# Performance work log

Measured on AMD Instinct MI355X. Metric: run time of the kernel, lower is better.

## Reference

```python
import jax, jax.numpy as jnp
import numpy as np

LN_EPS = 1e-5

def _layernorm(x, g, b):
    mu = jnp.mean(x, axis=-1, keepdims=True)
    var = jnp.var(x, axis=-1, keepdims=True)
    return (x - mu) * jax.lax.rsqrt(var + LN_EPS) * g + b

def setup_inputs() -> dict:
    key = jax.random.key(0)
    ks = jax.random.split(key, 8)
    B, N, C, OUT, H = 2, 512, 256, 256, 4
    s_in = 1.0 / np.sqrt(C)
    s_2c = 1.0 / np.sqrt(2 * C)
    s_out = 1.0 / np.sqrt(OUT)
    return {
        "x": jax.random.normal(ks[0], (B, N, C), jnp.float32),
        "We": jax.random.uniform(ks[1], (2 * C, OUT), jnp.float32, -s_2c, s_2c),
        "be": jnp.zeros((OUT,), jnp.float32),
        "ln1_g": jnp.ones((OUT,), jnp.float32),
        "ln1_b": jnp.zeros((OUT,), jnp.float32),
        "W2": jax.random.uniform(ks[2], (OUT, H), jnp.float32, -s_out, s_out),
        "b2": jnp.zeros((H,), jnp.float32),
        "Wv": jax.random.uniform(ks[3], (C, OUT), jnp.float32, -s_in, s_in),
        "bv": jnp.zeros((OUT,), jnp.float32),
        "Wo": jax.random.uniform(ks[4], (OUT, OUT), jnp.float32, -s_out, s_out),
        "bo": jnp.zeros((OUT,), jnp.float32),
        "ln2_g": jnp.ones((OUT,), jnp.float32),
        "ln2_b": jnp.zeros((OUT,), jnp.float32),
    }

def reference(x, We, be, ln1_g, ln1_b, W2, b2, Wv, bv, Wo, bo, ln2_g, ln2_b):
    B, N, C = x.shape
    OUT = We.shape[1]
    H = W2.shape[1]
    hd = OUT // H
    # edge MLP first Linear on concat([x_i, x_j]) == x_i@We[:C] + x_j@We[C:] + be
    h_i = x @ We[:C] + be          # [B,N,OUT]
    h_j = x @ We[C:]               # [B,N,OUT]
    e = h_i[:, :, None, :] + h_j[:, None, :, :]   # [B,Ni,Nj,OUT]
    e = jax.nn.gelu(_layernorm(e, ln1_g, ln1_b), approximate=False)
    logits = e @ W2 + b2                           # [B,Ni,Nj,H]
    adj = jax.nn.softmax(logits, axis=2)           # softmax over Nj
    v = (x @ Wv + bv).reshape(B, N, H, hd)         # [B,N,H,hd]
    out = jnp.einsum('bijh,bjhd->bihd', adj, v).reshape(B, N, OUT)
    out = out @ Wo + bo
    return _layernorm(out + x, ln2_g, ln2_b)
```

## Files before the change

kernel.cpp:

```cpp
#include <hip/hip_runtime.h>
#include <math.h>

#define NB    2
#define NN    512
#define CC    256
#define OUTC  256
#define HH    4
#define LN_EPS 1e-5f

__device__ __forceinline__ float gelu_fast(float x) {
    float s   = x * x;
    float w   = fmaf(-0.1029432f, s, -2.3022077f);
    float e   = exp2f(x * w);
    return x * __builtin_amdgcn_rcpf(1.0f + e);
}

__global__ __launch_bounds__(256) void kA(
    const float* __restrict__ x,  const float* __restrict__ We,
    const float* __restrict__ be, const float* __restrict__ Wv,
    const float* __restrict__ bv,
    float* __restrict__ hi, float* __restrict__ hj, float* __restrict__ v)
{
    __shared__ __align__(16) float xs[4][CC];
    const int r0 = blockIdx.x * 4;
    const int t  = threadIdx.x;
    #pragma unroll
    for (int k = 0; k < 4; ++k)
        xs[k][t] = x[(size_t)(r0 + k) * CC + t];
    __syncthreads();

    float ai[4] = {0,0,0,0}, aj[4] = {0,0,0,0}, av[4] = {0,0,0,0};
    for (int c = 0; c < CC; ++c) {
        float we0 = We[(size_t)c * OUTC + t];
        float we1 = We[(size_t)(CC + c) * OUTC + t];
        float wv  = Wv[(size_t)c * OUTC + t];
        #pragma unroll
        for (int k = 0; k < 4; ++k) {
            float xv = xs[k][c];
            ai[k] = fmaf(xv, we0, ai[k]);
            aj[k] = fmaf(xv, we1, aj[k]);
            av[k] = fmaf(xv, wv , av[k]);
        }
    }
    float beT = be[t], bvT = bv[t];
    #pragma unroll
    for (int k = 0; k < 4; ++k) {
        hi[(size_t)(r0 + k) * OUTC + t] = ai[k] + beT;
        hj[(size_t)(r0 + k) * OUTC + t] = aj[k];
        v [(size_t)(r0 + k) * OUTC + t] = av[k] + bvT;
    }
}

#define LDP 260
__global__ __launch_bounds__(256) void kB(
    const float* __restrict__ hi,  const float* __restrict__ hj,
    const float* __restrict__ ln1g, const float* __restrict__ ln1b,
    const float* __restrict__ W2,  const float* __restrict__ b2,
    float* __restrict__ logits)
{
    __shared__ __align__(16) float hjs[32][LDP];
    __shared__ __align__(16) float his[8][LDP];
    __shared__ __align__(16) float g1s[CC];
    __shared__ __align__(16) float b1s[CC];
    __shared__ __align__(16) float w2s[CC][HH];

    const int bid = blockIdx.x;
    const int jt  = (bid & 15) * 32;
    const int it  = ((bid >> 4) & 63) * 8;
    const int b   = bid >> 10;
    const int t   = threadIdx.x;

    {
        const float4* src = (const float4*)(hj + (size_t)(b * NN + jt) * OUTC);
        #pragma unroll
        for (int k = 0; k < 8; ++k) {
            int s   = k * 256 + t;
            int row = s >> 6, c4 = s & 63;
            *(float4*)&hjs[row][c4 * 4] = src[s];
        }
    }
    {
        const float4* src = (const float4*)(hi + (size_t)(b * NN + it) * OUTC);
        #pragma unroll
        for (int k = 0; k < 2; ++k) {
            int s   = k * 256 + t;
            int row = s >> 6, c4 = s & 63;
            *(float4*)&his[row][c4 * 4] = src[s];
        }
    }
    g1s[t] = ln1g[t];
    b1s[t] = ln1b[t];
    #pragma unroll
    for (int k = 0; k < 4; ++k)
        ((float*)w2s)[t + 256 * k] = W2[t + 256 * k];
    __syncthreads();

    const int w = t >> 6, l = t & 63;
    const int i = it + 2 * w + (l >> 5);
    const int j = jt + (l & 31);
    const float* __restrict__ hirow = &his[2 * w + (l >> 5)][0];
    const float* __restrict__ hjrow = &hjs[l & 31][0];

    float s = 0.f, ss = 0.f;
    #pragma unroll 4
    for (int c4 = 0; c4 < 64; ++c4) {
        float4 a  = *(const float4*)&hirow[c4 * 4];
        float4 bb = *(const float4*)&hjrow[c4 * 4];
        float e0 = a.x + bb.x, e1 = a.y + bb.y, e2 = a.z + bb.z, e3 = a.w + bb.w;
        s += (e0 + e1) + (e2 + e3);
        ss = fmaf(e0, e0, ss); ss = fmaf(e1, e1, ss);
        ss = fmaf(e2, e2, ss); ss = fmaf(e3, e3, ss);
    }
    const float mu  = s * (1.f / 256.f);
    const float var = fmaf(ss, 1.f / 256.f, -mu * mu);
    const float rs  = rsqrtf(var + LN_EPS);
    const float nmurs = -mu * rs;

    float p0 = 0.f, p1 = 0.f, p2 = 0.f, p3 = 0.f;
    #pragma unroll 4
    for (int c4 = 0; c4 < 64; ++c4) {
        float4 a  = *(const float4*)&hirow[c4 * 4];
        float4 bb = *(const float4*)&hjrow[c4 * 4];
        float4 g  = ((const float4*)g1s)[c4];
        float4 be_ = ((const float4*)b1s)[c4];
        const float4* w2r = (const float4*)&w2s[c4 * 4][0];
        {
            float n = fmaf(a.x + bb.x, rs, nmurs);
            n = fmaf(n, g.x, be_.x);
            float ge = gelu_fast(n);
            float4 wr = w2r[0];
            p0 = fmaf(ge, wr.x, p0); p1 = fmaf(ge, wr.y, p1);
            p2 = fmaf(ge, wr.z, p2); p3 = fmaf(ge, wr.w, p3);
        }
        {
            float n = fmaf(a.y + bb.y, rs, nmurs);
            n = fmaf(n, g.y, be_.y);
            float ge = gelu_fast(n);
            float4 wr = w2r[1];
            p0 = fmaf(ge, wr.x, p0); p1 = fmaf(ge, wr.y, p1);
            p2 = fmaf(ge, wr.z, p2); p3 = fmaf(ge, wr.w, p3);
        }
        {
            float n = fmaf(a.z + bb.z, rs, nmurs);
            n = fmaf(n, g.z, be_.z);
            float ge = gelu_fast(n);
            float4 wr = w2r[2];
            p0 = fmaf(ge, wr.x, p0); p1 = fmaf(ge, wr.y, p1);
            p2 = fmaf(ge, wr.z, p2); p3 = fmaf(ge, wr.w, p3);
        }
        {
            float n = fmaf(a.w + bb.w, rs, nmurs);
            n = fmaf(n, g.w, be_.w);
            float ge = gelu_fast(n);
            float4 wr = w2r[3];
            p0 = fmaf(ge, wr.x, p0); p1 = fmaf(ge, wr.y, p1);
            p2 = fmaf(ge, wr.z, p2); p3 = fmaf(ge, wr.w, p3);
        }
    }
    float4 b2v = *(const float4*)b2;
    float4 outv = make_float4(p0 + b2v.x, p1 + b2v.y, p2 + b2v.z, p3 + b2v.w);
    ((float4*)logits)[(size_t)(b * NN + i) * NN + j] = outv;
}

__global__ __launch_bounds__(256) void kC(
    const float* __restrict__ logits, const float* __restrict__ v,
    const float* __restrict__ Wo,     const float* __restrict__ bo,
    const float* __restrict__ x,      const float* __restrict__ g2,
    const float* __restrict__ b2ln,   float* __restrict__ out)
{
    __shared__ __align__(16) float wl[4 * NN * HH];
    __shared__ __align__(16) float sm[4][HH][2];
    __shared__ __align__(16) float out1[4][OUTC];
    __shared__ float redb[4][4][2];

    const int bid = blockIdx.x;
    const int b   = bid >> 7;
    const int it  = (bid & 127) * 4;
    const int t   = threadIdx.x;

    {
        const float4* src = (const float4*)logits + (size_t)(b * NN + it) * NN;
        float4* dst = (float4*)wl;
        #pragma unroll
        for (int k = 0; k < 8; ++k) dst[t + 256 * k] = src[t + 256 * k];
    }
    __syncthreads();

    {
        const int g = t >> 4, k = t & 15;
        const int i = g >> 2, h = g & 3;
        const float* base = wl + i * (NN * HH) + h;
        float m = -1e30f;
        for (int jj = 0; jj < 32; ++jj) m = fmaxf(m, base[(k * 32 + jj) * 4]);
        #pragma unroll
        for (int off = 1; off < 16; off <<= 1) m = fmaxf(m, __shfl_xor(m, off));
        float ssum = 0.f;
        for (int jj = 0; jj < 32; ++jj) ssum += __expf(base[(k * 32 + jj) * 4] - m);
        #pragma unroll
        for (int off = 1; off < 16; off <<= 1) ssum += __shfl_xor(ssum, off);
        if (k == 0) { sm[i][h][0] = m; sm[i][h][1] = 1.f / ssum; }
    }
    __syncthreads();

    {
        #pragma unroll 4
        for (int k = 0; k < 32; ++k) {
            int idx = t + 256 * k;
            int i = idx >> 11, h = idx & 3;
            wl[idx] = __expf(wl[idx] - sm[i][h][0]) * sm[i][h][1];
        }
    }
    __syncthreads();

    {
        const int h = t >> 6;
        float a0 = 0.f, a1 = 0.f, a2 = 0.f, a3 = 0.f;
        const float* vb = v + (size_t)b * NN * OUTC + t;
        for (int j = 0; j < NN; ++j) {
            float vv = vb[(size_t)j * OUTC];
            a0 = fmaf(wl[0 * 2048 + j * 4 + h], vv, a0);
            a1 = fmaf(wl[1 * 2048 + j * 4 + h], vv, a1);
            a2 = fmaf(wl[2 * 2048 + j * 4 + h], vv, a2);
            a3 = fmaf(wl[3 * 2048 + j * 4 + h], vv, a3);
        }
        out1[0][t] = a0; out1[1][t] = a1; out1[2][t] = a2; out1[3][t] = a3;
    }
    __syncthreads();

    {
        float a0 = bo[t], a1 = a0, a2 = a0, a3 = a0;
        for (int c = 0; c < OUTC; ++c) {
            float wv = Wo[(size_t)c * OUTC + t];
            a0 = fmaf(out1[0][c], wv, a0);
            a1 = fmaf(out1[1][c], wv, a1);
            a2 = fmaf(out1[2][c], wv, a2);
            a3 = fmaf(out1[3][c], wv, a3);
        }
        float r[4];
        r[0] = a0 + x[(size_t)(b * NN + it + 0) * OUTC + t];
        r[1] = a1 + x[(size_t)(b * NN + it + 1) * OUTC + t];
        r[2] = a2 + x[(size_t)(b * NN + it + 2) * OUTC + t];
        r[3] = a3 + x[(size_t)(b * NN + it + 3) * OUTC + t];

        const int w = t >> 6, l = t & 63;
        #pragma unroll
        for (int i = 0; i < 4; ++i) {
            float sv = r[i], sq = r[i] * r[i];
            #pragma unroll
            for (int off = 1; off < 64; off <<= 1) {
                sv += __shfl_xor(sv, off);
                sq += __shfl_xor(sq, off);
            }
            if (l == 0) { redb[w][i][0] = sv; redb[w][i][1] = sq; }
        }
        __syncthreads();
        float gg = g2[t], bb = b2ln[t];
        #pragma unroll
        for (int i = 0; i < 4; ++i) {
            float sv = redb[0][i][0] + redb[1][i][0] + redb[2][i][0] + redb[3][i][0];
            float sq = redb[0][i][1] + redb[1][i][1] + redb[2][i][1] + redb[3][i][1];
            float mu  = sv * (1.f / 256.f);
            float var = sq * (1.f / 256.f) - mu * mu;
            float rsi = rsqrtf(var + LN_EPS);
            out[(size_t)(b * NN + it + i) * OUTC + t] = (r[i] - mu) * rsi * gg + bb;
        }
    }
}

extern "C" void kernel_launch(void* const* d_in, const int* in_sizes, int n_in,
                              void* d_out, int out_size, void* d_ws, size_t ws_size,
                              hipStream_t stream) {
    (void)in_sizes; (void)n_in; (void)out_size; (void)ws_size;
    const float* x    = (const float*)d_in[0];
    const float* We   = (const float*)d_in[1];
    const float* be   = (const float*)d_in[2];
    const float* ln1g = (const float*)d_in[3];
    const float* ln1b = (const float*)d_in[4];
    const float* W2   = (const float*)d_in[5];
    const float* b2   = (const float*)d_in[6];
    const float* Wv   = (const float*)d_in[7];
    const float* bv   = (const float*)d_in[8];
    const float* Wo   = (const float*)d_in[9];
    const float* bo   = (const float*)d_in[10];
    const float* ln2g = (const float*)d_in[11];
    const float* ln2b = (const float*)d_in[12];
    float* out = (float*)d_out;

    float* ws = (float*)d_ws;
    float* hi     = ws;
    float* hj     = ws + 262144;
    float* v      = ws + 524288;
    float* logits = ws + 786432;

    kA<<<256,  256, 0, stream>>>(x, We, be, Wv, bv, hi, hj, v);
    kB<<<2048, 256, 0, stream>>>(hi, hj, ln1g, ln1b, W2, b2, logits);
    kC<<<256,  256, 0, stream>>>(logits, v, Wo, bo, x, ln2g, ln2b, out);
}
```

Measured before the change: 224.5 us.

## Decompose edge LayerNorm statistics into per-node sums plus cross dot-product kernel

The first-pass LayerNorm statistics in the edge kernel are no longer computed over all 256 channels per (i,j) pair. They are rebuilt algebraically from per-node sums and squared sums, emitted by kA, plus an hi·hj cross term produced by a new tiled dot-product kernel kX. This removes one full 256-wide pass per edge, at the cost of an extra launch, an extra workspace round trip, and possible cancellation in E[x^2]-mu^2. kA is also rewritten to give each wave one row with float4 weight loads, and kC now handles 2 rows per block so it launches twice as many blocks.

```diff
diff --git a/kernel.cpp b/kernel.cpp
--- a/kernel.cpp
+++ b/kernel.cpp
@@ -8,10 +8,20 @@
 #define HH    4
 #define LN_EPS 1e-5f
 
+#define WS_HI     0
+#define WS_HJ     262144
+#define WS_V      524288
+#define WS_LOGITS 786432
+#define WS_CROSS  2883584
+#define WS_SI     3407872
+#define WS_SSI    3408896
+#define WS_SJ     3409920
+#define WS_SSJ    3410944
+
 __device__ __forceinline__ float gelu_fast(float x) {
-    float s   = x * x;
-    float w   = fmaf(-0.1029432f, s, -2.3022077f);
-    float e   = exp2f(x * w);
+    float s = x * x;
+    float w = fmaf(-0.1029432f, s, -2.3022077f);
+    float e = exp2f(x * w);
     return x * __builtin_amdgcn_rcpf(1.0f + e);
 }
 
@@ -19,7 +29,9 @@
     const float* __restrict__ x,  const float* __restrict__ We,
     const float* __restrict__ be, const float* __restrict__ Wv,
     const float* __restrict__ bv,
-    float* __restrict__ hi, float* __restrict__ hj, float* __restrict__ v)
+    float* __restrict__ hi, float* __restrict__ hj, float* __restrict__ v,
+    float* __restrict__ Si, float* __restrict__ SSi,
+    float* __restrict__ Sj, float* __restrict__ SSj)
 {
     __shared__ __align__(16) float xs[4][CC];
     const int r0 = blockIdx.x * 4;
@@ -29,26 +41,97 @@
         xs[k][t] = x[(size_t)(r0 + k) * CC + t];
     __syncthreads();
 
-    float ai[4] = {0,0,0,0}, aj[4] = {0,0,0,0}, av[4] = {0,0,0,0};
+    const int w = t >> 6, l = t & 63;
+    const int r = r0 + w;
+    const float* __restrict__ xrow = xs[w];
+    const float4* __restrict__ We0 = (const float4*)We + l;
+    const float4* __restrict__ We1 = (const float4*)(We + (size_t)CC * OUTC) + l;
+    const float4* __restrict__ Wv4 = (const float4*)Wv + l;
+
+    float4 ai = {0,0,0,0}, aj = {0,0,0,0}, av = {0,0,0,0};
+    #pragma unroll 4
     for (int c = 0; c < CC; ++c) {
-        float we0 = We[(size_t)c * OUTC + t];
-        float we1 = We[(size_t)(CC + c) * OUTC + t];
-        float wv  = Wv[(size_t)c * OUTC + t];
-        #pragma unroll
-        for (int k = 0; k < 4; ++k) {
-            float xv = xs[k][c];
-            ai[k] = fmaf(xv, we0, ai[k]);
-            aj[k] = fmaf(xv, we1, aj[k]);
-            av[k] = fmaf(xv, wv , av[k]);
-        }
-    }
-    float beT = be[t], bvT = bv[t];
+        float xv = xrow[c];
+        float4 a = We0[(size_t)c * 64];
+        float4 bq = We1[(size_t)c * 64];
+        float4 cq = Wv4[(size_t)c * 64];
+        ai.x = fmaf(xv, a.x, ai.x); ai.y = fmaf(xv, a.y, ai.y);
+        ai.z = fmaf(xv, a.z, ai.z); ai.w = fmaf(xv, a.w, ai.w);
+        aj.x = fmaf(xv, bq.x, aj.x); aj.y = fmaf(xv, bq.y, aj.y);
+        aj.z = fmaf(xv, bq.z, aj.z); aj.w = fmaf(xv, bq.w, aj.w);
+        av.x = fmaf(xv, cq.x, av.x); av.y = fmaf(xv, cq.y, av.y);
+        av.z = fmaf(xv, cq.z, av.z); av.w = fmaf(xv, cq.w, av.w);
+    }
+    float4 be4 = ((const float4*)be)[l];
+    float4 bv4 = ((const float4*)bv)[l];
+    float4 hiv = make_float4(ai.x + be4.x, ai.y + be4.y, ai.z + be4.z, ai.w + be4.w);
+    float4 vv  = make_float4(av.x + bv4.x, av.y + bv4.y, av.z + bv4.z, av.w + bv4.w);
+
+    ((float4*)hi)[(size_t)r * 64 + l] = hiv;
+    ((float4*)hj)[(size_t)r * 64 + l] = aj;
+    ((float4*)v )[(size_t)r * 64 + l] = vv;
+
+    float si = (hiv.x + hiv.y) + (hiv.z + hiv.w);
+    float ssi = hiv.x * hiv.x;
+    ssi = fmaf(hiv.y, hiv.y, ssi); ssi = fmaf(hiv.z, hiv.z, ssi); ssi = fmaf(hiv.w, hiv.w, ssi);
+    float sj = (aj.x + aj.y) + (aj.z + aj.w);
+    float ssj = aj.x * aj.x;
+    ssj = fmaf(aj.y, aj.y, ssj); ssj = fmaf(aj.z, aj.z, ssj); ssj = fmaf(aj.w, aj.w, ssj);
     #pragma unroll
-    for (int k = 0; k < 4; ++k) {
-        hi[(size_t)(r0 + k) * OUTC + t] = ai[k] + beT;
-        hj[(size_t)(r0 + k) * OUTC + t] = aj[k];
-        v [(size_t)(r0 + k) * OUTC + t] = av[k] + bvT;
-    }
+    for (int off = 1; off < 64; off <<= 1) {
+        si  += __shfl_xor(si,  off);
+        ssi += __shfl_xor(ssi, off);
+        sj  += __shfl_xor(sj,  off);
+        ssj += __shfl_xor(ssj, off);
+    }
+    if (l == 0) { Si[r] = si; SSi[r] = ssi; Sj[r] = sj; SSj[r] = ssj; }
+}
+
+#define LXP 260
+__global__ __launch_bounds__(256) void kX(
+    const float* __restrict__ hi, const float* __restrict__ hj,
+    float* __restrict__ cross)
+{
+    __shared__ __align__(16) float his[32][LXP];
+    __shared__ __align__(16) float hjs[32][LXP];
+    const int bid = blockIdx.x;
+    const int b  = bid >> 8;
+    const int i0 = ((bid >> 4) & 15) * 32;
+    const int j0 = (bid & 15) * 32;
+    const int t  = threadIdx.x;
+
+    const float4* srcA = (const float4*)(hi + ((size_t)b * NN + i0) * OUTC);
+    const float4* srcB = (const float4*)(hj + ((size_t)b * NN + j0) * OUTC);
+    #pragma unroll
+    for (int k = 0; k < 8; ++k) {
+        int s = k * 256 + t, row = s >> 6, c4 = s & 63;
+        *(float4*)&his[row][c4 * 4] = srcA[s];
+        *(float4*)&hjs[row][c4 * 4] = srcB[s];
+    }
+    __syncthreads();
+
+    const int oi = (t & 15) * 2, oj = (t >> 4) * 2;
+    float a00 = 0.f, a01 = 0.f, a10 = 0.f, a11 = 0.f;
+    #pragma unroll 2
+    for (int c4 = 0; c4 < 64; ++c4) {
+        float4 A0 = *(const float4*)&his[oi    ][c4 * 4];
+        float4 A1 = *(const float4*)&his[oi + 1][c4 * 4];
+        float4 B0 = *(const float4*)&hjs[oj    ][c4 * 4];
+        float4 B1 = *(const float4*)&hjs[oj + 1][c4 * 4];
+        a00 = fmaf(A0.x, B0.x, a00); a00 = fmaf(A0.y, B0.y, a00);
+        a00 = fmaf(A0.z, B0.z, a00); a00 = fmaf(A0.w, B0.w, a00);
+        a01 = fmaf(A0.x, B1.x, a01); a01 = fmaf(A0.y, B1.y, a01);
+        a01 = fmaf(A0.z, B1.z, a01); a01 = fmaf(A0.w, B1.w, a01);
+        a10 = fmaf(A1.x, B0.x, a10); a10 = fmaf(A1.y, B0.y, a10);
+        a10 = fmaf(A1.z, B0.z, a10); a10 = fmaf(A1.w, B0.w, a10);
+        a11 = fmaf(A1.x, B1.x, a11); a11 = fmaf(A1.y, B1.y, a11);
+        a11 = fmaf(A1.z, B1.z, a11); a11 = fmaf(A1.w, B1.w, a11);
+    }
+    size_t base = ((size_t)b * NN + i0 + oi) * NN + j0 + oj;
+    cross[base]          = a00;
+    cross[base + 1]      = a01;
+    cross[base + NN]     = a10;
+    cross[base + NN + 1] = a11;
 }
 
 #define LDP 260
@@ -56,6 +139,9 @@
     const float* __restrict__ hi,  const float* __restrict__ hj,
     const float* __restrict__ ln1g, const float* __restrict__ ln1b,
     const float* __restrict__ W2,  const float* __restrict__ b2,
+    const float* __restrict__ Si,  const float* __restrict__ SSi,
+    const float* __restrict__ Sj,  const float* __restrict__ SSj,
+    const float* __restrict__ cross,
     float* __restrict__ logits)
 {
     __shared__ __align__(16) float hjs[32][LDP];
@@ -63,6 +149,8 @@
     __shared__ __align__(16) float g1s[CC];
     __shared__ __align__(16) float b1s[CC];
     __shared__ __align__(16) float w2s[CC][HH];
+    __shared__ __align__(16) float crs[256];
+    __shared__ float sis[8], ssis[8], sjs[32], ssjs[32];
 
     const int bid = blockIdx.x;
     const int jt  = (bid & 15) * 32;
@@ -74,8 +162,7 @@
         const float4* src = (const float4*)(hj + (size_t)(b * NN + jt) * OUTC);
         #pragma unroll
         for (int k = 0; k < 8; ++k) {
-            int s   = k * 256 + t;
-            int row = s >> 6, c4 = s & 63;
+            int s = k * 256 + t, row = s >> 6, c4 = s & 63;
             *(float4*)&hjs[row][c4 * 4] = src[s];
         }
     }
@@ -83,8 +170,7 @@
         const float4* src = (const float4*)(hi + (size_t)(b * NN + it) * OUTC);
         #pragma unroll
         for (int k = 0; k < 2; ++k) {
-            int s   = k * 256 + t;
-            int row = s >> 6, c4 = s & 63;
+            int s = k * 256 + t, row = s >> 6, c4 = s & 63;
             *(float4*)&his[row][c4 * 4] = src[s];
         }
     }
@@ -93,26 +179,22 @@
     #pragma unroll
     for (int k = 0; k < 4; ++k)
         ((float*)w2s)[t + 256 * k] = W2[t + 256 * k];
+    crs[t] = cross[((size_t)(b * NN + it + (t >> 5))) * NN + jt + (t & 31)];
+    if (t < 8)               { sis[t] = Si[b * NN + it + t];  ssis[t] = SSi[b * NN + it + t]; }
+    if (t >= 64 && t < 96)   { int q = t - 64; sjs[q] = Sj[b * NN + jt + q]; ssjs[q] = SSj[b * NN + jt + q]; }
     __syncthreads();
 
     const int w = t >> 6, l = t & 63;
-    const int i = it + 2 * w + (l >> 5);
-    const int j = jt + (l & 31);
-    const float* __restrict__ hirow = &his[2 * w + (l >> 5)][0];
-    const float* __restrict__ hjrow = &hjs[l & 31][0];
-
-    float s = 0.f, ss = 0.f;
-    #pragma unroll 4
-    for (int c4 = 0; c4 < 64; ++c4) {
-        float4 a  = *(const float4*)&hirow[c4 * 4];
-        float4 bb = *(const float4*)&hjrow[c4 * 4];
-        float e0 = a.x + bb.x, e1 = a.y + bb.y, e2 = a.z + bb.z, e3 = a.w + bb.w;
-        s += (e0 + e1) + (e2 + e3);
-        ss = fmaf(e0, e0, ss); ss = fmaf(e1, e1, ss);
-        ss = fmaf(e2, e2, ss); ss = fmaf(e3, e3, ss);
-    }
-    const float mu  = s * (1.f / 256.f);
-    const float var = fmaf(ss, 1.f / 256.f, -mu * mu);
+    const int il = 2 * w + (l >> 5);
+    const int jl = l & 31;
+    const int i = it + il;
+    const int j = jt + jl;
+    const float* __restrict__ hirow = &his[il][0];
+    const float* __restrict__ hjrow = &hjs[jl][0];
+
+    const float mu  = (sis[il] + sjs[jl]) * (1.f / 256.f);
+    const float msq = fmaf(2.f, crs[(il << 5) + jl], ssis[il] + ssjs[jl]) * (1.f / 256.f);
+    const float var = fmaf(-mu, mu, msq);
     const float rs  = rsqrtf(var + LN_EPS);
     const float nmurs = -mu * rs;
 
@@ -168,101 +250,108 @@
     const float* __restrict__ x,      const float* __restrict__ g2,
     const float* __restrict__ b2ln,   float* __restrict__ out)
 {
-    __shared__ __align__(16) float wl[4 * NN * HH];
-    __shared__ __align__(16) float sm[4][HH][2];
-    __shared__ __align__(16) float out1[4][OUTC];
-    __shared__ float redb[4][4][2];
+    __shared__ __align__(16) float wl[2][NN * HH];
+    __shared__ __align__(16) float sm[2][HH][2];
+    __shared__ __align__(16) float out1[2][OUTC];
+    __shared__ float redb[4][2][2];
 
     const int bid = blockIdx.x;
-    const int b   = bid >> 7;
-    const int it  = (bid & 127) * 4;
+    const int b   = bid >> 8;
+    const int i0  = (bid & 255) * 2;
     const int t   = threadIdx.x;
 
     {
-        const float4* src = (const float4*)logits + (size_t)(b * NN + it) * NN;
+        const float4* src = (const float4*)(logits + ((size_t)b * NN + i0) * NN * HH);
         float4* dst = (float4*)wl;
         #pragma unroll
-        for (int k = 0; k < 8; ++k) dst[t + 256 * k] = src[t + 256 * k];
-    }
-    __syncthreads();
-
-    {
-        const int g = t >> 4, k = t & 15;
-        const int i = g >> 2, h = g & 3;
-        const float* base = wl + i * (NN * HH) + h;
+        for (int k = 0; k < 4; ++k) dst[k * 256 + t] = src[k * 256 + t];
+    }
+    __syncthreads();
+
+    {
+        const int g = t >> 5, k = t & 31;
+        const int row = g >> 2, h = g & 3;
+        const float* base = wl[row] + h;
         float m = -1e30f;
-        for (int jj = 0; jj < 32; ++jj) m = fmaxf(m, base[(k * 32 + jj) * 4]);
-        #pragma unroll
-        for (int off = 1; off < 16; off <<= 1) m = fmaxf(m, __shfl_xor(m, off));
+        #pragma unroll
+        for (int mm = 0; mm < 16; ++mm) m = fmaxf(m, base[(k + 32 * mm) * 4]);
+        #pragma unroll
+        for (int off = 1; off < 32; off <<= 1) m = fmaxf(m, __shfl_xor(m, off, 32));
         float ssum = 0.f;
-        for (int jj = 0; jj < 32; ++jj) ssum += __expf(base[(k * 32 + jj) * 4] - m);
-        #pragma unroll
-        for (int off = 1; off < 16; off <<= 1) ssum += __shfl_xor(ssum, off);
-        if (k == 0) { sm[i][h][0] = m; sm[i][h][1] = 1.f / ssum; }
-    }
-    __syncthreads();
-
-    {
+        #pragma unroll
+        for (int mm = 0; mm < 16; ++mm) ssum += __expf(base[(k + 32 * mm) * 4] - m);
+        #pragma unroll
+        for (int off = 1; off < 32; off <<= 1) ssum += __shfl_xor(ssum, off, 32);
+        if (k == 0) { sm[row][h][0] = m; sm[row][h][1] = 1.f / ssum; }
+    }
+    __syncthreads();
+
+    {
+        float* wlf = &wl[0][0];
         #pragma unroll 4
-        for (int k = 0; k < 32; ++k) {
+        for (int k = 0; k < 16; ++k) {
             int idx = t + 256 * k;
-            int i = idx >> 11, h = idx & 3;
-            wl[idx] = __expf(wl[idx] - sm[i][h][0]) * sm[i][h][1];
+            int row = idx >> 11, h = idx & 3;
+            wlf[idx] = __expf(wlf[idx] - sm[row][h][0]) * sm[row][h][1];
         }
     }
     __syncthreads();
 
     {
         const int h = t >> 6;
-        float a0 = 0.f, a1 = 0.f, a2 = 0.f, a3 = 0.f;
+        float a0 = 0.f, a1 = 0.f;
         const float* vb = v + (size_t)b * NN * OUTC + t;
+        const float* p0 = wl[0] + h;
+        const float* p1 = wl[1] + h;
+        #pragma unroll 8
         for (int j = 0; j < NN; ++j) {
             float vv = vb[(size_t)j * OUTC];
-            a0 = fmaf(wl[0 * 2048 + j * 4 + h], vv, a0);
-            a1 = fmaf(wl[1 * 2048 + j * 4 + h], vv, a1);
-            a2 = fmaf(wl[2 * 2048 + j * 4 + h], vv, a2);
-            a3 = fmaf(wl[3 * 2048 + j * 4 + h], vv, a3);
-        }
-        out1[0][t] = a0; out1[1][t] = a1; out1[2][t] = a2; out1[3][t] = a3;
-    }
-    __syncthreads();
-
-    {
-        float a0 = bo[t], a1 = a0, a2 = a0, a3 = a0;
+            a0 = fmaf(p0[j * 4], vv, a0);
+            a1 = fmaf(p1[j * 4], vv, a1);
+        }
+        out1[0][t] = a0; out1[1][t] = a1;
+    }
+    __syncthreads();
+
+    {
+        float a0 = bo[t], a1 = a0;
+        #pragma unroll 4
         for (int c = 0; c < OUTC; ++c) {
             float wv = Wo[(size_t)c * OUTC + t];
             a0 = fmaf(out1[0][c], wv, a0);
             a1 = fmaf(out1[1][c], wv, a1);
-            a2 = fmaf(out1[2][c], wv, a2);
-            a3 = fmaf(out1[3][c], wv, a3);
-        }
-        float r[4];
-        r[0] = a0 + x[(size_t)(b * NN + it + 0) * OUTC + t];
-        r[1] = a1 + x[(size_t)(b * NN + it + 1) * OUTC + t];
-        r[2] = a2 + x[(size_t)(b * NN + it + 2) * OUTC + t];
-        r[3] = a3 + x[(size_t)(b * NN + it + 3) * OUTC + t];
+        }
+        float r0v = a0 + x[((size_t)b * NN + i0    ) * OUTC + t];
+        float r1v = a1 + x[((size_t)b * NN + i0 + 1) * OUTC + t];
 
         const int w = t >> 6, l = t & 63;
-        #pragma unroll
-        for (int i = 0; i < 4; ++i) {
-            float sv = r[i], sq = r[i] * r[i];
-            #pragma unroll
-            for (int off = 1; off < 64; off <<= 1) {
-                sv += __shfl_xor(sv, off);
-                sq += __shfl_xor(sq, off);
-            }
-            if (l == 0) { redb[w][i][0] = sv; redb[w][i][1] = sq; }
+        float sv0 = r0v, sq0 = r0v * r0v, sv1 = r1v, sq1 = r1v * r1v;
+        #pragma unroll
+        for (int off = 1; off < 64; off <<= 1) {
+            sv0 += __shfl_xor(sv0, off); sq0 += __shfl_xor(sq0, off);
+            sv1 += __shfl_xor(sv1, off); sq1 += __shfl_xor(sq1, off);
+        }
+        if (l == 0) {
+            redb[w][0][0] = sv0; redb[w][0][1] = sq0;
+            redb[w][1][0] = sv1; redb[w][1][1] = sq1;
         }
         __syncthreads();
         float gg = g2[t], bb = b2ln[t];
-        #pragma unroll
-        for (int i = 0; i < 4; ++i) {
-            float sv = redb[0][i][0] + redb[1][i][0] + redb[2][i][0] + redb[3][i][0];
-            float sq = redb[0][i][1] + redb[1][i][1] + redb[2][i][1] + redb[3][i][1];
-            float mu  = sv * (1.f / 256.f);
+        {
+            float sv = redb[0][0][0] + redb[1][0][0] + redb[2][0][0] + redb[3][0][0];
+            float sq = redb[0][0][1] + redb[1][0][1] + redb[2][0][1] + redb[3][0][1];
+            float mu = sv * (1.f / 256.f);
             float var = sq * (1.f / 256.f) - mu * mu;
             float rsi = rsqrtf(var + LN_EPS);
-            out[(size_t)(b * NN + it + i) * OUTC + t] = (r[i] - mu) * rsi * gg + bb;
+            out[((size_t)b * NN + i0) * OUTC + t] = (r0v - mu) * rsi * gg + bb;
+        }
+        {
+            float sv = redb[0][1][0] + redb[1][1][0] + redb[2][1][0] + redb[3][1][0];
+            float sq = redb[0][1][1] + redb[1][1][1] + redb[2][1][1] + redb[3][1][1];
+            float mu = sv * (1.f / 256.f);
+            float var = sq * (1.f / 256.f) - mu * mu;
+            float rsi = rsqrtf(var + LN_EPS);
+            out[((size_t)b * NN + i0 + 1) * OUTC + t] = (r1v - mu) * rsi * gg + bb;
         }
     }
 }
@@ -287,12 +376,19 @@
     float* out = (float*)d_out;
 
     float* ws = (float*)d_ws;
-    float* hi     = ws;
-    float* hj     = ws + 262144;
-    float* v      = ws + 524288;
-    float* logits = ws + 786432;
-
-    kA<<<256,  256, 0, stream>>>(x, We, be, Wv, bv, hi, hj, v);
-    kB<<<2048, 256, 0, stream>>>(hi, hj, ln1g, ln1b, W2, b2, logits);
-    kC<<<256,  256, 0, stream>>>(logits, v, Wo, bo, x, ln2g, ln2b, out);
-}
+    float* hi     = ws + WS_HI;
+    float* hj     = ws + WS_HJ;
+    float* v      = ws + WS_V;
+    float* logits = ws + WS_LOGITS;
+    float* cross  = ws + WS_CROSS;
+    float* Si     = ws + WS_SI;
+    float* SSi    = ws + WS_SSI;
+    float* Sj     = ws + WS_SJ;
+    float* SSj    = ws + WS_SSJ;
+
+    kA<<<256,  256, 0, stream>>>(x, We, be, Wv, bv, hi, hj, v, Si, SSi, Sj, SSj);
+    kX<<<512,  256, 0, stream>>>(hi, hj, cross);
+    kB<<<2048, 256, 0, stream>>>(hi, hj, ln1g, ln1b, W2, b2,
+                                 Si, SSi, Sj, SSj, cross, logits);
+    kC<<<512,  256, 0, stream>>>(logits, v, Wo, bo, x, ln2g, ln2b, out);
+}
```

Measured after the change: 241.6 us. 7.6% more time.
